# Kernel optimization log

Hardware: AMD Instinct MI355X
Metric: run time of the kernel (lower is better)

The kernel has to match this reference:

```python
import jax, jax.numpy as jnp
import numpy as np

# ---- config (mirrors init_kwargs) ----
D_MODEL = 1024
D_STATE = 128
EXPAND = 2
HEADDIM = 64
D_INNER = D_MODEL * EXPAND            # 2048
NHEADS = D_INNER // HEADDIM           # 32
ROPE_FRACTION = 0.5
ROTATE_DIM = (int(D_STATE * ROPE_FRACTION) // 2) * 2   # 64
NUM_ANGLES = ROTATE_DIM // 2          # 32
A_FLOOR = 1e-4
EPS = 1e-5
IN_PROJ_DIM = 2 * D_INNER + 2 * D_STATE + 3 * NHEADS + NUM_ANGLES  # 4480
BATCH, SEQLEN = 2, 2048


def _state_rmsnorm(x, w):
    rms = jnp.sqrt(jnp.mean(x * x, axis=-1, keepdims=True) + EPS)
    return x / rms * w


def _apply_rotary_pairs(x, phase):
    # x: (b,s,h,d_state), phase: (b,s,h,num_pairs)
    if ROTATE_DIM == 0:
        return x
    x_rot = x[..., :ROTATE_DIM].reshape(*x.shape[:-1], ROTATE_DIM // 2, 2)
    x_pass = x[..., ROTATE_DIM:]
    cos = jnp.cos(phase)
    sin = jnp.sin(phase)
    real = x_rot[..., 0]
    imag = x_rot[..., 1]
    rr = real * cos - imag * sin
    ri = real * sin + imag * cos
    rotated = jnp.stack([rr, ri], axis=-1).reshape(*x.shape[:-1], ROTATE_DIM)
    if x_pass.shape[-1] == 0:
        return rotated
    return jnp.concatenate([rotated, x_pass], axis=-1)


def setup_inputs() -> dict:
    key = jax.random.key(0)
    ks = jax.random.split(key, 5)
    x = jax.random.normal(ks[0], (BATCH, SEQLEN, D_MODEL), jnp.float32)
    W_in = jax.random.normal(ks[1], (IN_PROJ_DIM, D_MODEL), jnp.float32) / np.sqrt(D_MODEL)
    # dt_bias ~ inverse-softplus of dt sampled in [dt_min, dt_max]
    dt = jnp.exp(jax.random.uniform(ks[2], (NHEADS,), jnp.float32) * (np.log(0.1) - np.log(0.001)) + np.log(0.001))
    dt = jnp.clip(dt, 1e-4)
    dt_bias = dt + jnp.log(-jnp.expm1(-dt))
    B_norm_w = jnp.ones((D_STATE,), jnp.float32)
    C_norm_w = jnp.ones((D_STATE,), jnp.float32)
    B_bias = jnp.ones((NHEADS, D_STATE), jnp.float32)
    C_bias = jnp.ones((NHEADS, D_STATE), jnp.float32)
    D_param = jnp.ones((NHEADS,), jnp.float32)
    out_norm_w = jnp.ones((D_INNER,), jnp.float32)
    W_out = jax.random.normal(ks[3], (D_MODEL, D_INNER), jnp.float32) / np.sqrt(D_INNER)
    return {"x": x, "W_in": W_in, "dt_bias": dt_bias, "B_norm_w": B_norm_w,
            "C_norm_w": C_norm_w, "B_bias": B_bias, "C_bias": C_bias,
            "D_param": D_param, "out_norm_w": out_norm_w, "W_out": W_out}


def reference(x, W_in, dt_bias, B_norm_w, C_norm_w, B_bias, C_bias, D_param, out_norm_w, W_out):
    b, s, _ = x.shape
    proj = jnp.einsum('bsd,pd->bsp', x, W_in)
    sizes = [D_INNER, D_INNER, D_STATE, D_STATE, NHEADS, NHEADS, NHEADS, NUM_ANGLES]
    offs = np.cumsum([0] + sizes)
    z, v, B_raw, C_raw, dd_dt, dd_A, trap_logits, angle_logits = [
        proj[..., offs[i]:offs[i + 1]] for i in range(8)]
    z = z.reshape(b, s, NHEADS, HEADDIM)
    v = v.reshape(b, s, NHEADS, HEADDIM)
    Bm = _state_rmsnorm(B_raw, B_norm_w)[:, :, None, :] + B_bias[None, None]   # (b,s,h,n)
    Cm = _state_rmsnorm(C_raw, C_norm_w)[:, :, None, :] + C_bias[None, None]
    dt = jax.nn.softplus(dd_dt + dt_bias[None, None])          # (b,s,h)
    A = jnp.minimum(-jax.nn.softplus(dd_A), -A_FLOOR)          # (b,s,h)
    trap = jax.nn.sigmoid(trap_logits)                          # (b,s,h)
    phase = jnp.cumsum(angle_logits, axis=1)[:, :, None, :]     # (b,s,1,angles)
    phase = jnp.broadcast_to(phase, (b, s, NHEADS, NUM_ANGLES))
    Bm = _apply_rotary_pairs(Bm, phase)
    Cm = _apply_rotary_pairs(Cm, phase)

    alpha = jnp.exp(A * dt)               # (b,s,h)
    beta = (1.0 - trap) * dt * alpha
    gamma = trap * dt

    # move time to leading for scan: (s, b, h, ...)
    def tl(a):
        return jnp.moveaxis(a, 1, 0)
    xs = (tl(alpha), tl(beta), tl(gamma), tl(Bm), tl(Cm), tl(v))

    state0 = jnp.zeros((b, NHEADS, HEADDIM, D_STATE), jnp.float32)
    pk0 = jnp.zeros((b, NHEADS, D_STATE), jnp.float32)
    pv0 = jnp.zeros((b, NHEADS, HEADDIM), jnp.float32)

    def step(carry, inp):
        state, pk, pv = carry
        a_t, b_t, g_t, k_t, q_t, v_t = inp
        prev_outer = pv[..., :, None] * pk[..., None, :]        # (b,h,p,n)
        curr_outer = v_t[..., :, None] * k_t[..., None, :]
        state = (a_t[..., None, None] * state
                 + b_t[..., None, None] * prev_outer
                 + g_t[..., None, None] * curr_outer)
        y_t = jnp.einsum('bhpn,bhn->bhp', state, q_t) + D_param[None, :, None] * v_t
        return (state, k_t, v_t), y_t

    _, ys = jax.lax.scan(step, (state0, pk0, pv0), xs)
    y = jnp.moveaxis(ys, 0, 1).reshape(b, s, D_INNER)
    z = z.reshape(b, s, D_INNER)
    # GatedRMSNorm
    rms = jnp.sqrt(jnp.mean(y * y, axis=-1, keepdims=True) + EPS)
    y = (y / rms * out_norm_w) * jax.nn.silu(z)
    return jnp.einsum('bsi,di->bsd', y, W_out)
```

## Files before the change

### kernel.cpp

```cpp
#include <hip/hip_runtime.h>
#include <math.h>

#define S_LEN 2048
#define NBATCH 2
#define DMODEL 1024
#define PDIM 4480
#define DI 2048
#define NH 32
#define HD 64
#define DS 128
#define NA 32
#define CHK 64
#define NC (S_LEN / CHK)
#define ZV 4096
#define PS 384
#define PS_B 0
#define PS_C 128
#define PS_DT 256
#define PS_A 288
#define PS_TRAP 320
#define PS_ANG 352

typedef __attribute__((ext_vector_type(8))) short s8v;
typedef __attribute__((ext_vector_type(4))) float f4v;

__device__ __forceinline__ float softplus_f(float x) {
    return x > 20.f ? x : log1pf(expf(x));
}

__device__ __forceinline__ ushort f2bf(float f) {
    unsigned u = __float_as_uint(f);
    unsigned r = (u + 0x7fffu + ((u >> 16) & 1u)) >> 16;
    return (ushort)r;
}

__device__ __forceinline__ uint4 pack8(const float* f) {
    uint4 o;
    o.x = (unsigned)f2bf(f[0]) | ((unsigned)f2bf(f[1]) << 16);
    o.y = (unsigned)f2bf(f[2]) | ((unsigned)f2bf(f[3]) << 16);
    o.z = (unsigned)f2bf(f[4]) | ((unsigned)f2bf(f[5]) << 16);
    o.w = (unsigned)f2bf(f[6]) | ((unsigned)f2bf(f[7]) << 16);
    return o;
}

__device__ __forceinline__ float bf2f(ushort u) {
    return __uint_as_float(((unsigned)u) << 16);
}
__device__ __forceinline__ float bf_lo(unsigned u) { return __uint_as_float(u << 16); }
__device__ __forceinline__ float bf_hi(unsigned u) { return __uint_as_float(u & 0xffff0000u); }

__device__ __forceinline__ void unpack8(uint4 a, float* f) {
    f[0] = bf_lo(a.x); f[1] = bf_hi(a.x);
    f[2] = bf_lo(a.y); f[3] = bf_hi(a.y);
    f[4] = bf_lo(a.z); f[5] = bf_hi(a.z);
    f[6] = bf_lo(a.w); f[7] = bf_hi(a.w);
}

#define NCX  524288
#define NCWI 573440
#define NCWO 262144
__global__ __launch_bounds__(256)
void f2bf_all(const float* __restrict__ x, const float* __restrict__ wi,
              const float* __restrict__ wo, ushort* __restrict__ xbf,
              ushort* __restrict__ wibf, ushort* __restrict__ wobf) {
    int idx = blockIdx.x * 256 + threadIdx.x;
    const float* src; ushort* dst; int shift, rel;
    if (idx < NCX)              { rel = idx;               src = x;  dst = xbf;  shift = 7; }
    else if (idx < NCX + NCWI)  { rel = idx - NCX;         src = wi; dst = wibf; shift = 7; }
    else                        { rel = idx - NCX - NCWI;  src = wo; dst = wobf; shift = 8; }
    int dc = rel ^ ((rel >> shift) & 7);
    const float* ip = src + (size_t)rel * 8;
    float4 v0 = *(const float4*)ip;
    float4 v1 = *(const float4*)(ip + 4);
    uint4 o;
    o.x = (unsigned)f2bf(v0.x) | ((unsigned)f2bf(v0.y) << 16);
    o.y = (unsigned)f2bf(v0.z) | ((unsigned)f2bf(v0.w) << 16);
    o.z = (unsigned)f2bf(v1.x) | ((unsigned)f2bf(v1.y) << 16);
    o.w = (unsigned)f2bf(v1.z) | ((unsigned)f2bf(v1.w) << 16);
    *(uint4*)(dst + (size_t)dc * 8) = o;
}

__global__ __launch_bounds__(256, 2)
void gemm_bf16(const ushort* __restrict__ A, const ushort* __restrict__ B,
               float* __restrict__ Cf, ushort* __restrict__ Cb,
               int M, int N, int K, int split, int fstride) {
    __shared__ __align__(16) short lA[128 * 64];
    __shared__ __align__(16) short lB[128 * 64];
    int nwg = gridDim.x;
    int bid = blockIdx.x;
    int q = nwg >> 3;
    int swz = (bid & 7) * q + (bid >> 3);
    int nb = N >> 7;
    int bx = swz % nb, by = swz / nb;

    int tid = threadIdx.x;
    int wv = tid >> 6, ln = tid & 63;
    int rl = ln & 15, kg = ln >> 4, r7 = rl & 7;
    int R0 = (wv >> 1) * 64, C0 = (wv & 1) * 64;

    const ushort* Ag = A + (size_t)(by * 128 + wv * 32 + (ln >> 3)) * K + (ln & 7) * 8;
    const ushort* Bg = B + (size_t)(bx * 128 + wv * 32 + (ln >> 3)) * K + (ln & 7) * 8;
    short* lAw = lA + (wv * 32) * 64;
    short* lBw = lB + (wv * 32) * 64;

    f4v acc[4][4];
#pragma unroll
    for (int m = 0; m < 4; ++m)
#pragma unroll
        for (int n = 0; n < 4; ++n) acc[m][n] = f4v{0.f, 0.f, 0.f, 0.f};

    for (int k0 = 0; k0 < K; k0 += 64) {
        __syncthreads();
#pragma unroll
        for (int i = 0; i < 4; ++i) {
            __builtin_amdgcn_global_load_lds(
                (const __attribute__((address_space(1))) void*)(Ag + (size_t)i * 8 * K + k0),
                (__attribute__((address_space(3))) void*)(lAw + i * 8 * 64), 16, 0, 0);
            __builtin_amdgcn_global_load_lds(
                (const __attribute__((address_space(1))) void*)(Bg + (size_t)i * 8 * K + k0),
                (__attribute__((address_space(3))) void*)(lBw + i * 8 * 64), 16, 0, 0);
        }
        __syncthreads();
#pragma unroll
        for (int ks = 0; ks < 2; ++ks) {
            int kc = ks * 4 + kg;
            int co = ((kc ^ r7) << 3);
            s8v av[4], bv[4];
#pragma unroll
            for (int m = 0; m < 4; ++m)
                av[m] = *(const s8v*)&lA[(R0 + m * 16 + rl) * 64 + co];
#pragma unroll
            for (int n = 0; n < 4; ++n)
                bv[n] = *(const s8v*)&lB[(C0 + n * 16 + rl) * 64 + co];
#pragma unroll
            for (int m = 0; m < 4; ++m)
#pragma unroll
                for (int n = 0; n < 4; ++n)
                    acc[m][n] = __builtin_amdgcn_mfma_f32_16x16x32_bf16(
                        av[m], bv[n], acc[m][n], 0, 0, 0);
        }
    }
    if (bx * 128 < split) {
#pragma unroll
        for (int m = 0; m < 4; ++m)
#pragma unroll
            for (int n = 0; n < 4; ++n) {
                size_t row0 = (size_t)(by * 128 + R0 + m * 16 + kg * 4);
                int col = bx * 128 + C0 + n * 16 + rl;
#pragma unroll
                for (int r = 0; r < 4; ++r)
                    Cb[(row0 + r) * split + col] = f2bf(acc[m][n][r]);
            }
    } else {
#pragma unroll
        for (int m = 0; m < 4; ++m)
#pragma unroll
            for (int n = 0; n < 4; ++n) {
                size_t row0 = (size_t)(by * 128 + R0 + m * 16 + kg * 4);
                int col = bx * 128 + C0 + n * 16 + rl - split;
#pragma unroll
                for (int r = 0; r < 4; ++r)
                    Cf[(row0 + r) * fstride + col] = acc[m][n][r];
            }
    }
}

__global__ __launch_bounds__(256)
void phase_kernel(const float* __restrict__ projS, float* __restrict__ cosb,
                  float* __restrict__ sinb) {
    int b = blockIdx.x >> 5;
    int j = blockIdx.x & 31;
    int tid = threadIdx.x;
    __shared__ float part[256];
    float v[8];
    float run = 0.f;
#pragma unroll
    for (int e = 0; e < 8; ++e) {
        int s = tid * 8 + e;
        v[e] = projS[((size_t)(b * S_LEN + s)) * PS + PS_ANG + j];
        run += v[e];
    }
    part[tid] = run;
    __syncthreads();
    for (int off = 1; off < 256; off <<= 1) {
        float add = (tid >= off) ? part[tid - off] : 0.f;
        __syncthreads();
        part[tid] += add;
        __syncthreads();
    }
    float acc = (tid > 0) ? part[tid - 1] : 0.f;
#pragma unroll
    for (int e = 0; e < 8; ++e) {
        acc += v[e];
        int s = tid * 8 + e;
        size_t o = ((size_t)(b * S_LEN + s)) * NA + j;
        cosb[o] = cosf(acc);
        sinb[o] = sinf(acc);
    }
}

__global__ __launch_bounds__(128)
void prep_kernel(const float* __restrict__ projS, const float* __restrict__ dt_bias,
                 const float* __restrict__ Bw, const float* __restrict__ Cw,
                 const float* __restrict__ cosb, const float* __restrict__ sinb,
                 float* __restrict__ Bn, float* __restrict__ Cn,
                 float* __restrict__ ldb, float* __restrict__ wbuf,
                 float* __restrict__ pubuf) {
    size_t row = blockIdx.x;
    int b = (int)(row >> 11);
    int s = (int)(row & 2047);
    int n = threadIdx.x;
    const float* pr = projS + row * PS;
    float vB = pr[PS_B + n];
    float vC = pr[PS_C + n];
    float sB = vB * vB, sC = vC * vC;
#pragma unroll
    for (int off = 32; off >= 1; off >>= 1) {
        sB += __shfl_xor(sB, off);
        sC += __shfl_xor(sC, off);
    }
    __shared__ float redB[2], redC[2];
    if ((n & 63) == 0) { redB[n >> 6] = sB; redC[n >> 6] = sC; }
    __syncthreads();
    float rB = sqrtf((redB[0] + redB[1]) * (1.f / 128.f) + 1e-5f);
    float rC = sqrtf((redC[0] + redC[1]) * (1.f / 128.f) + 1e-5f);
    float bn = vB / rB * Bw[n];
    float cn = vC / rC * Cw[n];
    float bp = __shfl_xor(bn, 1);
    float cp = __shfl_xor(cn, 1);
    float ob = bn, oc = cn;
    if (n < 64) {
        float c = cosb[row * NA + (n >> 1)];
        float sn_ = sinb[row * NA + (n >> 1)];
        if ((n & 1) == 0) { ob = bn * c - bp * sn_; oc = cn * c - cp * sn_; }
        else              { ob = bp * sn_ + bn * c; oc = cp * sn_ + cn * c; }
    }
    Bn[row * DS + n] = ob;
    Cn[row * DS + n] = oc;
    if (n < NH) {
        int h = n;
        float dtv = softplus_f(pr[PS_DT + h] + dt_bias[h]);
        float Av = -fmaxf(softplus_f(pr[PS_A + h]), 1e-4f);
        float trap = 1.f / (1.f + expf(-pr[PS_TRAP + h]));
        size_t o = ((size_t)(b * NH + h)) * S_LEN + s;
        ldb[o]   = Av * dtv;
        wbuf[o]  = trap * dtv;
        pubuf[o] = (1.f - trap) * dtv;
    }
}

__global__ __launch_bounds__(256)
void lcum_kernel(float* __restrict__ ell) {
    size_t row = blockIdx.x;
    int tid = threadIdx.x;
    float* p = ell + row * S_LEN;
    float v[8];
    float run = 0.f;
#pragma unroll
    for (int e = 0; e < 8; ++e) { v[e] = p[tid * 8 + e]; run += v[e]; }
    __shared__ float part[256];
    part[tid] = run;
    __syncthreads();
    for (int off = 1; off < 256; off <<= 1) {
        float add = (tid >= off) ? part[tid - off] : 0.f;
        __syncthreads();
        part[tid] += add;
        __syncthreads();
    }
    float acc = (tid > 0) ? part[tid - 1] : 0.f;
#pragma unroll
    for (int e = 0; e < 8; ++e) { acc += v[e]; p[tid * 8 + e] = acc; }
}

__device__ __forceinline__ void build32v(
    float* vals, const float* __restrict__ br, const float* __restrict__ bias,
    const float* __restrict__ cr, const float* __restrict__ sr, int rot) {
    float bv[32], bi[32];
#pragma unroll
    for (int j = 0; j < 8; ++j) *(float4*)&bv[j * 4] = *(const float4*)(br + j * 4);
#pragma unroll
    for (int j = 0; j < 8; ++j) *(float4*)&bi[j * 4] = *(const float4*)(bias + j * 4);
    if (rot) {
        float cf[16], sf[16];
#pragma unroll
        for (int j = 0; j < 4; ++j) {
            *(float4*)&cf[j * 4] = *(const float4*)(cr + j * 4);
            *(float4*)&sf[j * 4] = *(const float4*)(sr + j * 4);
        }
#pragma unroll
        for (int a = 0; a < 16; ++a) {
            float c = cf[a], s = sf[a], e = bi[2 * a], o = bi[2 * a + 1];
            vals[2 * a]     = bv[2 * a]     + e * c - o * s;
            vals[2 * a + 1] = bv[2 * a + 1] + e * s + o * c;
        }
    } else {
#pragma unroll
        for (int j = 0; j < 32; ++j) vals[j] = bv[j] + bi[j];
    }
}

__global__ __launch_bounds__(256, 4)
void delta_kernel(const ushort* __restrict__ zvbf, const float* __restrict__ Bn,
                  const float* __restrict__ cosb, const float* __restrict__ sinb,
                  const float* __restrict__ ell, const float* __restrict__ wbuf,
                  const float* __restrict__ pubuf, const float* __restrict__ B_bias,
                  ushort* __restrict__ dstate, ushort* __restrict__ vtbuf,
                  ushort* __restrict__ kbuf, float* __restrict__ rbuf) {
    __shared__ __align__(16) ushort KT[DS * CHK];
    __shared__ __align__(16) ushort cVT[HD * CHK];
    __shared__ __align__(16) ushort VT[HD * CHK];
    int blk = blockIdx.x;
    int c = blk & (NC - 1);
    int h = (blk >> 5) & (NH - 1);
    int b = blk >> 10;
    int tid = threadIdx.x;
    size_t row0 = (size_t)b * S_LEN + c * CHK;
    size_t bh = (size_t)b * NH + h;
    int i = tid >> 2, q4 = tid & 3;

    size_t so = bh * S_LEN + c * CHK + i;
    float llast = ell[bh * S_LEN + c * CHK + CHK - 1];
    float li = ell[so];
    float u = wbuf[so];
    if (c * CHK + i < S_LEN - 1) u += pubuf[so + 1];
    float coef = expf(llast - li) * u;
    if (tid == 0) {
        float base = (c == 0) ? 0.f : ell[bh * S_LEN + c * CHK - 1];
        rbuf[blk] = expf(llast - base);
    }
    {
        int n0 = q4 * 32;
        float vals[32];
        build32v(vals, Bn + (row0 + i) * DS + n0, B_bias + h * DS + n0,
                 cosb + (row0 + i) * NA + q4 * 16, sinb + (row0 + i) * NA + q4 * 16,
                 q4 < 2);
#pragma unroll
        for (int j = 0; j < 32; ++j) {
            int n = n0 + j;
            KT[n * 64 + (((i >> 3) ^ (n & 7)) << 3) + (i & 7)] = f2bf(vals[j]);
        }
        ushort* kd = kbuf + (size_t)blk * (CHK * DS);
#pragma unroll
        for (int j = 0; j < 4; ++j) {
            int cc = (q4 * 4 + j) ^ (i & 7);
            *(uint4*)&kd[i * 128 + cc * 8] = pack8(&vals[j * 8]);
        }
    }
    {
        int p0 = q4 * 16;
        const ushort* vp = zvbf + (size_t)(row0 + i) * ZV + 2048 + h * HD + p0;
        uint4 a0 = *(const uint4*)vp;
        uint4 a1 = *(const uint4*)(vp + 8);
        unsigned uu[8] = {a0.x, a0.y, a0.z, a0.w, a1.x, a1.y, a1.z, a1.w};
#pragma unroll
        for (int j = 0; j < 8; ++j) {
            ushort v0 = (ushort)(uu[j] & 0xffffu);
            ushort v1 = (ushort)(uu[j] >> 16);
            int p = p0 + 2 * j;
            int addr0 = p * 64 + (((i >> 3) ^ (p & 7)) << 3) + (i & 7);
            int addr1 = (p + 1) * 64 + (((i >> 3) ^ ((p + 1) & 7)) << 3) + (i & 7);
            VT[addr0]  = v0;
            VT[addr1]  = v1;
            cVT[addr0] = f2bf(bf2f(v0) * coef);
            cVT[addr1] = f2bf(bf2f(v1) * coef);
        }
    }
    __syncthreads();
    {
        const uint4* vs = (const uint4*)VT;
        uint4* vd = (uint4*)(vtbuf + (size_t)blk * (HD * CHK));
        vd[tid] = vs[tid];
        vd[tid + 256] = vs[tid + 256];
    }
    int wv = tid >> 6, ln = tid & 63, rl = ln & 15, kg = ln >> 4;
    int pA = wv * 16 + rl;
    s8v aV[2];
#pragma unroll
    for (int ks = 0; ks < 2; ++ks)
        aV[ks] = *(const s8v*)&cVT[pA * 64 + (((ks * 4 + kg) ^ (pA & 7)) << 3)];
    ushort* dp = dstate + (size_t)blk * (HD * DS);
#pragma unroll
    for (int nt = 0; nt < 8; ++nt) {
        int nB = nt * 16 + rl;
        f4v dacc = f4v{0.f, 0.f, 0.f, 0.f};
#pragma unroll
        for (int ks = 0; ks < 2; ++ks) {
            s8v bK = *(const s8v*)&KT[nB * 64 + (((ks * 4 + kg) ^ (nB & 7)) << 3)];
            dacc = __builtin_amdgcn_mfma_f32_16x16x32_bf16(aV[ks], bK, dacc, 0, 0, 0);
        }
#pragma unroll
        for (int r = 0; r < 4; ++r) {
            int p = wv * 16 + kg * 4 + r;
            int n = nt * 16 + rl;
            dp[p * DS + (((n >> 3) ^ (p & 7)) << 3) + (n & 7)] = f2bf(dacc[r]);
        }
    }
}

__global__ __launch_bounds__(256)
void state_prop(ushort* __restrict__ dstate, const float* __restrict__ rbuf) {
    size_t bh = blockIdx.x;
    int tid = threadIdx.x;
    float st[32];
#pragma unroll
    for (int j = 0; j < 32; ++j) st[j] = 0.f;
    uint4* base = (uint4*)dstate;
    size_t b0 = bh * NC * 1024ull;
    uint4 nxt[4];
#pragma unroll
    for (int j = 0; j < 4; ++j) nxt[j] = base[b0 + tid * 4 + j];
    for (int c = 0; c < NC; ++c) {
        uint4 cur[4];
#pragma unroll
        for (int j = 0; j < 4; ++j) cur[j] = nxt[j];
        if (c + 1 < NC) {
#pragma unroll
            for (int j = 0; j < 4; ++j)
                nxt[j] = base[b0 + (size_t)(c + 1) * 1024 + tid * 4 + j];
        }
        float r = rbuf[bh * NC + c];
        uint4 outv[4];
#pragma unroll
        for (int j = 0; j < 4; ++j) {
            unsigned uu[4] = {cur[j].x, cur[j].y, cur[j].z, cur[j].w};
            unsigned oo[4];
#pragma unroll
            for (int e = 0; e < 4; ++e) {
                float d0 = bf_lo(uu[e]), d1 = bf_hi(uu[e]);
                int ix = j * 8 + e * 2;
                oo[e] = (unsigned)f2bf(st[ix]) | ((unsigned)f2bf(st[ix + 1]) << 16);
                st[ix]     = fmaf(r, st[ix], d0);
                st[ix + 1] = fmaf(r, st[ix + 1], d1);
            }
            outv[j] = uint4{oo[0], oo[1], oo[2], oo[3]};
        }
#pragma unroll
        for (int j = 0; j < 4; ++j)
            base[b0 + (size_t)c * 1024 + tid * 4 + j] = outv[j];
    }
}

__global__ __launch_bounds__(256, 4)
void out_kernel(const float* __restrict__ Cn, const float* __restrict__ cosb,
                const float* __restrict__ sinb, const float* __restrict__ ell,
                const float* __restrict__ wbuf, const float* __restrict__ pubuf,
                const float* __restrict__ C_bias, const ushort* __restrict__ dstate,
                const ushort* __restrict__ vtbuf, const ushort* __restrict__ kbuf,
                float* __restrict__ yb) {
    __shared__ __align__(16) ushort Qb[CHK * DS];
    __shared__ __align__(16) ushort Kb[CHK * DS];
    __shared__ __align__(16) ushort VTb[HD * CHK];
    int blk = blockIdx.x;
    int c = blk & (NC - 1);
    int h = (blk >> 5) & (NH - 1);
    int b = blk >> 10;
    int tid = threadIdx.x;
    size_t row0 = (size_t)b * S_LEN + c * CHK;
    size_t bh = (size_t)b * NH + h;
    int i = tid >> 2, q4 = tid & 3;
    int wv2 = tid >> 6, ln = tid & 63;

    {
        const ushort* kg_ = kbuf + (size_t)blk * (CHK * DS);
#pragma unroll
        for (int k = 0; k < 4; ++k) {
            int ch = wv2 * 256 + k * 64;
            __builtin_amdgcn_global_load_lds(
                (const __attribute__((address_space(1))) void*)(kg_ + (size_t)(ch + ln) * 8),
                (__attribute__((address_space(3))) void*)(Kb + ch * 8), 16, 0, 0);
        }
        const ushort* vg = vtbuf + (size_t)blk * (HD * CHK);
#pragma unroll
        for (int k = 0; k < 2; ++k) {
            int ch = wv2 * 128 + k * 64;
            __builtin_amdgcn_global_load_lds(
                (const __attribute__((address_space(1))) void*)(vg + (size_t)(ch + ln) * 8),
                (__attribute__((address_space(3))) void*)(VTb + ch * 8), 16, 0, 0);
        }
    }
    {
        int n0 = q4 * 32;
        float vals[32];
        build32v(vals, Cn + (row0 + i) * DS + n0, C_bias + h * DS + n0,
                 cosb + (row0 + i) * NA + q4 * 16, sinb + (row0 + i) * NA + q4 * 16,
                 q4 < 2);
#pragma unroll
        for (int j = 0; j < 4; ++j) {
            int cc = (q4 * 4 + j) ^ (i & 7);
            *(uint4*)&Qb[i * 128 + cc * 8] = pack8(&vals[j * 8]);
        }
    }
    __syncthreads();

    int rl = ln & 15, kg = ln >> 4;
    int tA = wv2 * 16 + rl;
    s8v aQ[4];
#pragma unroll
    for (int kc = 0; kc < 4; ++kc)
        aQ[kc] = *(const s8v*)&Qb[tA * 128 + (((kc * 4 + kg) ^ (tA & 7)) << 3)];
    f4v pacc[4];
#pragma unroll
    for (int st = 0; st < 4; ++st) pacc[st] = f4v{0.f, 0.f, 0.f, 0.f};
#pragma unroll
    for (int st = 0; st < 4; ++st) {
        int sB = st * 16 + rl;
#pragma unroll
        for (int kc = 0; kc < 4; ++kc) {
            s8v bK = *(const s8v*)&Kb[sB * 128 + (((kc * 4 + kg) ^ (sB & 7)) << 3)];
            pacc[st] = __builtin_amdgcn_mfma_f32_16x16x32_bf16(aQ[kc], bK, pacc[st], 0, 0, 0);
        }
    }
    __syncthreads();

    {
        const ushort* sg = dstate + (size_t)blk * (CHK * DS);
#pragma unroll
        for (int k = 0; k < 4; ++k) {
            int ch = wv2 * 256 + k * 64;
            __builtin_amdgcn_global_load_lds(
                (const __attribute__((address_space(1))) void*)(sg + (size_t)(ch + ln) * 8),
                (__attribute__((address_space(3))) void*)(Kb + ch * 8), 16, 0, 0);
        }
    }
    size_t so0 = bh * S_LEN + c * CHK;
    float basev = (c == 0) ? 0.f : ell[so0 - 1];
    int t2r0 = wv2 * 16 + kg * 4;
    float et[4], wr[4];
#pragma unroll
    for (int r = 0; r < 4; ++r) {
        size_t so = so0 + t2r0 + r;
        et[r] = expf(ell[so] - basev);
        wr[r] = wbuf[so];
    }
    float fs[4];
#pragma unroll
    for (int st = 0; st < 4; ++st) {
        int s = st * 16 + rl;
        size_t sos = so0 + s;
        float u = wbuf[sos];
        if (c * CHK + s < S_LEN - 1) u += pubuf[sos + 1];
        fs[st] = u * expf(fminf(basev - ell[sos], 80.f));
    }
    ushort* PTb = Qb;
#pragma unroll
    for (int st = 0; st < 4; ++st) {
        int s = st * 16 + rl;
#pragma unroll
        for (int r = 0; r < 4; ++r) {
            int t2 = t2r0 + r;
            float m;
            if (s < t2)       m = et[r] * fs[st];
            else if (s == t2) m = wr[r];
            else              m = 0.f;
            PTb[t2 * 64 + (((s >> 3) ^ (t2 & 7)) << 3) + (s & 7)] = f2bf(pacc[st][r] * m);
        }
    }
    __syncthreads();

    s8v aP[2];
#pragma unroll
    for (int ks = 0; ks < 2; ++ks)
        aP[ks] = *(const s8v*)&PTb[tA * 64 + (((ks * 4 + kg) ^ (tA & 7)) << 3)];
    f4v y1[4], y2[4];
#pragma unroll
    for (int pt = 0; pt < 4; ++pt) { y1[pt] = f4v{0.f,0.f,0.f,0.f}; y2[pt] = f4v{0.f,0.f,0.f,0.f}; }
#pragma unroll
    for (int pt = 0; pt < 4; ++pt) {
        int pB = pt * 16 + rl;
#pragma unroll
        for (int ks = 0; ks < 2; ++ks) {
            s8v bV = *(const s8v*)&VTb[pB * 64 + (((ks * 4 + kg) ^ (pB & 7)) << 3)];
            y1[pt] = __builtin_amdgcn_mfma_f32_16x16x32_bf16(aP[ks], bV, y1[pt], 0, 0, 0);
        }
#pragma unroll
        for (int kc = 0; kc < 4; ++kc) {
            s8v bS = *(const s8v*)&Kb[pB * 128 + (((kc * 4 + kg) ^ (pB & 7)) << 3)];
            y2[pt] = __builtin_amdgcn_mfma_f32_16x16x32_bf16(aQ[kc], bS, y2[pt], 0, 0, 0);
        }
    }
    float* yp = yb + (size_t)blk * (CHK * HD);
#pragma unroll
    for (int pt = 0; pt < 4; ++pt) {
#pragma unroll
        for (int r = 0; r < 4; ++r) {
            int t2 = t2r0 + r;
            int p = pt * 16 + rl;
            yp[t2 * HD + p] = y1[pt][r] + et[r] * y2[pt][r];
        }
    }
}

__global__ __launch_bounds__(256)
void ynorm_kernel(const float* __restrict__ yb, const ushort* __restrict__ zvbf,
                  const float* __restrict__ w, const float* __restrict__ D_param,
                  ushort* __restrict__ ybf) {
    size_t row = blockIdx.x;
    int b = (int)(row >> 11);
    int s = (int)(row & 2047);
    int c = s >> 6, t = s & 63;
    int tid = threadIdx.x;
    int hh = tid >> 3;
    int p0 = (tid * 8) & 63;
    const float* yr = yb + (((size_t)(b * NH + hh) * NC + c) * CHK + t) * HD + p0;
    float4 v0 = *(const float4*)yr;
    float4 v1 = *(const float4*)(yr + 4);
    float vvf[8];
    unpack8(*(const uint4*)(zvbf + row * (size_t)ZV + 2048 + tid * 8), vvf);
    float Dp = D_param[hh];
    float yv[8] = {v0.x + Dp * vvf[0], v0.y + Dp * vvf[1], v0.z + Dp * vvf[2], v0.w + Dp * vvf[3],
                   v1.x + Dp * vvf[4], v1.y + Dp * vvf[5], v1.z + Dp * vvf[6], v1.w + Dp * vvf[7]};
    float ss = 0.f;
#pragma unroll
    for (int e = 0; e < 8; ++e) ss += yv[e] * yv[e];
#pragma unroll
    for (int off = 32; off >= 1; off >>= 1) ss += __shfl_xor(ss, off);
    __shared__ float red[4];
    if ((tid & 63) == 0) red[tid >> 6] = ss;
    __syncthreads();
    float tot = red[0] + red[1] + red[2] + red[3];
    float rinv = 1.f / sqrtf(tot * (1.f / 2048.f) + 1e-5f);
    float zv[8];
    unpack8(*(const uint4*)(zvbf + row * (size_t)ZV + tid * 8), zv);
    float4 w0 = *(const float4*)(w + tid * 8);
    float4 w1 = *(const float4*)(w + tid * 8 + 4);
    float wv[8] = {w0.x, w0.y, w0.z, w0.w, w1.x, w1.y, w1.z, w1.w};
    ushort u[8];
#pragma unroll
    for (int e = 0; e < 8; ++e) {
        float sil = zv[e] / (1.f + expf(-zv[e]));
        u[e] = f2bf(yv[e] * rinv * wv[e] * sil);
    }
    int dstc = (tid & ~7) | ((tid & 7) ^ ((int)row & 7));
    uint4 o;
    o.x = (unsigned)u[0] | ((unsigned)u[1] << 16);
    o.y = (unsigned)u[2] | ((unsigned)u[3] << 16);
    o.z = (unsigned)u[4] | ((unsigned)u[5] << 16);
    o.w = (unsigned)u[6] | ((unsigned)u[7] << 16);
    *(uint4*)(ybf + row * (size_t)DI + dstc * 8) = o;
}

extern "C" void kernel_launch(void* const* d_in, const int* in_sizes, int n_in,
                              void* d_out, int out_size, void* d_ws, size_t ws_size,
                              hipStream_t stream) {
    const float* x          = (const float*)d_in[0];
    const float* W_in       = (const float*)d_in[1];
    const float* dt_bias    = (const float*)d_in[2];
    const float* B_norm_w   = (const float*)d_in[3];
    const float* C_norm_w   = (const float*)d_in[4];
    const float* B_bias     = (const float*)d_in[5];
    const float* C_bias     = (const float*)d_in[6];
    const float* D_param    = (const float*)d_in[7];
    const float* out_norm_w = (const float*)d_in[8];
    const float* W_out      = (const float*)d_in[9];
    float* out = (float*)d_out;

    const size_t M = (size_t)NBATCH * S_LEN;
    const size_t NBLK = (size_t)NBATCH * NH * NC;
    float* ws = (float*)d_ws;
    size_t off = 0;
    float* projS = ws + off; off += M * PS;
    float* cosb  = ws + off; off += M * NA;
    float* sinb  = ws + off; off += M * NA;
    float* Bn    = ws + off; off += M * DS;
    float* Cn    = ws + off; off += M * DS;
    float* ell   = ws + off; off += (size_t)NBATCH * NH * S_LEN;
    float* wbuf  = ws + off; off += (size_t)NBATCH * NH * S_LEN;
    float* pubuf = ws + off; off += (size_t)NBATCH * NH * S_LEN;
    float* yb    = ws + off; off += NBLK * CHK * HD;
    float* rbuf  = ws + off; off += NBLK;
    ushort* zvbf = (ushort*)(ws + off); off += M * ZV / 2;
    ushort* xbf  = (ushort*)(ws + off); off += M * DMODEL / 2;
    ushort* wibf = (ushort*)(ws + off); off += (size_t)PDIM * DMODEL / 2;
    ushort* wobf = (ushort*)(ws + off); off += (size_t)DMODEL * DI / 2;
    ushort* ybf  = (ushort*)(ws + off); off += M * DI / 2;
    ushort* dstate = (ushort*)(ws + off); off += NBLK * CHK * DS / 2;
    ushort* vtbuf  = (ushort*)(ws + off); off += NBLK * HD * CHK / 2;
    ushort* kbuf   = (ushort*)(ws + off); off += NBLK * CHK * DS / 2;

    f2bf_all<<<dim3((NCX + NCWI + NCWO) / 256), 256, 0, stream>>>(
        x, W_in, W_out, xbf, wibf, wobf);
    gemm_bf16<<<dim3((PDIM / 128) * (int)(M / 128)), 256, 0, stream>>>(
        xbf, wibf, projS, zvbf, (int)M, PDIM, DMODEL, ZV, PS);
    phase_kernel<<<dim3(NBATCH * NA), 256, 0, stream>>>(projS, cosb, sinb);
    prep_kernel<<<dim3((int)M), 128, 0, stream>>>(projS, dt_bias, B_norm_w, C_norm_w,
                                                  cosb, sinb, Bn, Cn, ell, wbuf, pubuf);
    lcum_kernel<<<dim3(NBATCH * NH), 256, 0, stream>>>(ell);
    delta_kernel<<<dim3((int)NBLK), 256, 0, stream>>>(zvbf, Bn, cosb, sinb, ell,
                                                      wbuf, pubuf, B_bias, dstate,
                                                      vtbuf, kbuf, rbuf);
    state_prop<<<dim3(NBATCH * NH), 256, 0, stream>>>(dstate, rbuf);
    out_kernel<<<dim3((int)NBLK), 256, 0, stream>>>(Cn, cosb, sinb, ell,
                                                    wbuf, pubuf, C_bias,
                                                    dstate, vtbuf, kbuf, yb);
    ynorm_kernel<<<dim3((int)M), 256, 0, stream>>>(yb, zvbf, out_norm_w, D_param, ybf);
    gemm_bf16<<<dim3((DMODEL / 128) * (int)(M / 128)), 256, 0, stream>>>(
        ybf, wobf, out, nullptr, (int)M, DMODEL, DI, 0, DMODEL);
}
```

Before: 242.3 us.

## Split state propagation across 4x more blocks and add supertile GEMM block mapping

The chunk-state propagation kernel now launches four blocks per (batch, head) instead of one. Each thread carries 8 state values instead of 32, which raises parallelism and memory-level concurrency for this serial scan over chunks. Separately, the GEMM maps blocks onto 4-row by SW-column supertiles (SW=5 for in_proj, 4 for out_proj) to improve L2 reuse of A and B tiles. The supertile mapping assumes the tile-column count divides by SW (35/5 and 8/4 hold) and the row count divides by 4.

```diff
diff --git a/kernel.cpp b/kernel.cpp
--- a/kernel.cpp
+++ b/kernel.cpp
@@ -83,15 +83,19 @@
 __global__ __launch_bounds__(256, 2)
 void gemm_bf16(const ushort* __restrict__ A, const ushort* __restrict__ B,
                float* __restrict__ Cf, ushort* __restrict__ Cb,
-               int M, int N, int K, int split, int fstride) {
+               int M, int N, int K, int split, int fstride, int SW) {
     __shared__ __align__(16) short lA[128 * 64];
     __shared__ __align__(16) short lB[128 * 64];
     int nwg = gridDim.x;
     int bid = blockIdx.x;
-    int q = nwg >> 3;
-    int swz = (bid & 7) * q + (bid >> 3);
+    int chunk = nwg >> 3;
+    int swz = (bid & 7) * chunk + (bid >> 3);
     int nb = N >> 7;
-    int bx = swz % nb, by = swz / nb;
+    int sup = 4 * SW;
+    int st = swz / sup, w = swz % sup;
+    int stPerRow = nb / SW;
+    int by = (st / stPerRow) * 4 + w / SW;
+    int bx = (st % stPerRow) * SW + w % SW;
 
     int tid = threadIdx.x;
     int wv = tid >> 6, ln = tid & 63;
@@ -399,44 +403,31 @@
 
 __global__ __launch_bounds__(256)
 void state_prop(ushort* __restrict__ dstate, const float* __restrict__ rbuf) {
-    size_t bh = blockIdx.x;
+    int g = blockIdx.x;
+    size_t bh = (size_t)(g >> 2);
+    int sl = g & 3;
     int tid = threadIdx.x;
-    float st[32];
-#pragma unroll
-    for (int j = 0; j < 32; ++j) st[j] = 0.f;
+    float st[8];
+#pragma unroll
+    for (int j = 0; j < 8; ++j) st[j] = 0.f;
     uint4* base = (uint4*)dstate;
-    size_t b0 = bh * NC * 1024ull;
-    uint4 nxt[4];
-#pragma unroll
-    for (int j = 0; j < 4; ++j) nxt[j] = base[b0 + tid * 4 + j];
+    size_t off0 = bh * NC * 1024ull + (size_t)sl * 256 + tid;
+    uint4 nxt = base[off0];
     for (int c = 0; c < NC; ++c) {
-        uint4 cur[4];
-#pragma unroll
-        for (int j = 0; j < 4; ++j) cur[j] = nxt[j];
-        if (c + 1 < NC) {
-#pragma unroll
-            for (int j = 0; j < 4; ++j)
-                nxt[j] = base[b0 + (size_t)(c + 1) * 1024 + tid * 4 + j];
-        }
+        uint4 cur = nxt;
+        if (c + 1 < NC) nxt = base[off0 + (size_t)(c + 1) * 1024];
         float r = rbuf[bh * NC + c];
-        uint4 outv[4];
-#pragma unroll
-        for (int j = 0; j < 4; ++j) {
-            unsigned uu[4] = {cur[j].x, cur[j].y, cur[j].z, cur[j].w};
-            unsigned oo[4];
-#pragma unroll
-            for (int e = 0; e < 4; ++e) {
-                float d0 = bf_lo(uu[e]), d1 = bf_hi(uu[e]);
-                int ix = j * 8 + e * 2;
-                oo[e] = (unsigned)f2bf(st[ix]) | ((unsigned)f2bf(st[ix + 1]) << 16);
-                st[ix]     = fmaf(r, st[ix], d0);
-                st[ix + 1] = fmaf(r, st[ix + 1], d1);
-            }
-            outv[j] = uint4{oo[0], oo[1], oo[2], oo[3]};
-        }
-#pragma unroll
-        for (int j = 0; j < 4; ++j)
-            base[b0 + (size_t)c * 1024 + tid * 4 + j] = outv[j];
+        unsigned uu[4] = {cur.x, cur.y, cur.z, cur.w};
+        unsigned oo[4];
+#pragma unroll
+        for (int e = 0; e < 4; ++e) {
+            float d0 = bf_lo(uu[e]), d1 = bf_hi(uu[e]);
+            int ix = e * 2;
+            oo[e] = (unsigned)f2bf(st[ix]) | ((unsigned)f2bf(st[ix + 1]) << 16);
+            st[ix]     = fmaf(r, st[ix], d0);
+            st[ix + 1] = fmaf(r, st[ix + 1], d1);
+        }
+        base[off0 + (size_t)c * 1024] = uint4{oo[0], oo[1], oo[2], oo[3]};
     }
 }
 
@@ -680,7 +671,7 @@
     f2bf_all<<<dim3((NCX + NCWI + NCWO) / 256), 256, 0, stream>>>(
         x, W_in, W_out, xbf, wibf, wobf);
     gemm_bf16<<<dim3((PDIM / 128) * (int)(M / 128)), 256, 0, stream>>>(
-        xbf, wibf, projS, zvbf, (int)M, PDIM, DMODEL, ZV, PS);
+        xbf, wibf, projS, zvbf, (int)M, PDIM, DMODEL, ZV, PS, 5);
     phase_kernel<<<dim3(NBATCH * NA), 256, 0, stream>>>(projS, cosb, sinb);
     prep_kernel<<<dim3((int)M), 128, 0, stream>>>(projS, dt_bias, B_norm_w, C_norm_w,
                                                   cosb, sinb, Bn, Cn, ell, wbuf, pubuf);
@@ -688,11 +679,11 @@
     delta_kernel<<<dim3((int)NBLK), 256, 0, stream>>>(zvbf, Bn, cosb, sinb, ell,
                                                       wbuf, pubuf, B_bias, dstate,
                                                       vtbuf, kbuf, rbuf);
-    state_prop<<<dim3(NBATCH * NH), 256, 0, stream>>>(dstate, rbuf);
+    state_prop<<<dim3(NBATCH * NH * 4), 256, 0, stream>>>(dstate, rbuf);
     out_kernel<<<dim3((int)NBLK), 256, 0, stream>>>(Cn, cosb, sinb, ell,
                                                     wbuf, pubuf, C_bias,
                                                     dstate, vtbuf, kbuf, yb);
     ynorm_kernel<<<dim3((int)M), 256, 0, stream>>>(yb, zvbf, out_norm_w, D_param, ybf);
     gemm_bf16<<<dim3((DMODEL / 128) * (int)(M / 128)), 256, 0, stream>>>(
-        ybf, wobf, out, nullptr, (int)M, DMODEL, DI, 0, DMODEL);
-}
+        ybf, wobf, out, nullptr, (int)M, DMODEL, DI, 0, DMODEL, 4);
+}
```

New measurement: 219.9 us. 1.1x faster.
